# Kernel tuning notes

Measured on AMD Instinct MI355X. Metric: run time of the kernel, lower is better.

Reference implementation:

```python
import jax, jax.numpy as jnp
import numpy as np

N_AA = 20          # size of 'ACDEFGHIKLMNPQRSTVWY'
GAP = 20           # gap token; one_hot maps it to an all-zero row (matches '-' skipping)
N_SEQS, SEQ_LEN = 2048, 512
MAX_MI_POS = 100   # min(seq_len, 100) in the source
PSEUDOCOUNT = 0.01


def _features(msa, pc):
    n_seqs, seq_len = msa.shape
    pseudocount = PSEUDOCOUNT * pc[0]

    # one-hot encode; tokens >= N_AA (gaps / unknown) become zero rows,
    # exactly matching the 'if aa in self.aa_to_idx' / "aa != '-'" skips.
    oh = jax.nn.one_hot(msa, N_AA, dtype=jnp.float32)          # [N, L, 20]

    # ---- PSSM ----
    counts = oh.sum(0)                                          # [L, 20]
    freq = (counts + pseudocount) / (n_seqs + pseudocount * N_AA)
    pssm = jnp.log(freq * N_AA + 1e-10)                         # log(freq / (1/20) + 1e-10)

    # ---- Conservation (Shannon entropy over non-gap residues) ----
    total = counts.sum(-1, keepdims=True)                       # [L, 1] non-gap count
    f = counts / jnp.maximum(total, 1.0)
    # f == 0 terms contribute 0 * log2(1e-10) == 0, matching dict-based skipping
    entropy = -(f * jnp.log2(f + 1e-10)).sum(-1)                # [L]
    conservation = jnp.where(total[:, 0] > 0,
                             1.0 - entropy / np.log2(N_AA), 0.0)

    # ---- Mutual information over the first M positions ----
    M = min(seq_len, MAX_MI_POS)
    ohm = oh[:, :M, :]                                          # [N, M, 20]
    # joint counts over sequences where BOTH positions are non-gap
    J = jnp.einsum('nia,njb->ijab', ohm, ohm)                   # [M, M, 20, 20]
    tot = J.sum((2, 3))                                         # [M, M]
    tot_safe = jnp.maximum(tot, 1.0)
    p = J / tot_safe[:, :, None, None]                          # joint prob p_ij
    pi = p.sum(3)[:, :, :, None]                                # marginal p_i (pair-conditioned)
    pj = p.sum(2)[:, :, None, :]                                # marginal p_j
    denom = jnp.maximum(pi * pj, 1e-30)
    term = jnp.where(J > 0, p * jnp.log2(p / denom + 1e-10), 0.0)
    mi = jnp.where(tot > 0, term.sum((2, 3)), 0.0)              # [M, M]
    mi = mi * (1.0 - jnp.eye(M, dtype=mi.dtype))                # diagonal left at 0
    mi_matrix = jnp.zeros((seq_len, seq_len), jnp.float32).at[:M, :M].set(mi)

    return pssm, conservation, mi_matrix


def setup_inputs() -> dict:
    key = jax.random.key(0)
    k1, _ = jax.random.split(key)
    # tokens 0..19 = amino acids, 20 = gap '-'
    msa = jax.random.randint(k1, (N_SEQS, SEQ_LEN), 0, N_AA + 1, dtype=jnp.int32)
    pc = jnp.ones((1,), dtype=jnp.float32)  # pseudocount scale (==1 -> pseudocount 0.01)
    return {"msa": msa, "pc": pc}


def reference(msa, pc):
    return _features(msa, pc)
```

## Files before the change

kernel.cpp:

```cpp
#include <hip/hip_runtime.h>

#define N_SEQS 2048
#define SEQ_LEN 512
#define NAA 20
#define NS 21
#define MPOS 100
#define G 4
#define NG (MPOS / G)
#define NTILE (NG * (NG + 1) / 2)
#define POSB (SEQ_LEN / 8)
#define HBINS (NS * NS)

__global__ __launch_bounds__(256) void fused_kernel(const int* __restrict__ msa,
                                                    const float* __restrict__ pc,
                                                    float* __restrict__ pssm,
                                                    float* __restrict__ cons,
                                                    float* __restrict__ mi) {
    __shared__ int h_s[16 * HBINS];
    __shared__ float ra_s[4][NAA], cb_s[4][NAA];

    const int tid = threadIdx.x;
    const int w = tid >> 6;
    const int lane = tid & 63;
    const int bid = blockIdx.x;

    if (bid < NTILE) {
        int t = bid, ti = 0, off = 0;
        while (off + (NG - ti) <= t) { off += NG - ti; ++ti; }
        const int tj = ti + (t - off);
        const int i0 = ti * G, j0 = tj * G;
        const bool diag = (ti == tj);

        for (int k = tid; k < 16 * HBINS; k += 256) h_s[k] = 0;
        __syncthreads();

#pragma unroll
        for (int k = 0; k < 8; ++k) {
            const int s = tid + (k << 8);
            const int* rp = msa + (size_t)s * SEQ_LEN;
            const int4 va = *(const int4*)(rp + i0);
            const int4 vb = *(const int4*)(rp + j0);
            const int A0 = va.x * 21, A1 = va.y * 21, A2 = va.z * 21, A3 = va.w * 21;
            const int B0 = vb.x, B1 = vb.y, B2 = vb.z, B3 = vb.w;
            atomicAdd(&h_s[0 * 1764 + 0 * 441 + A0 + B0], 1);
            atomicAdd(&h_s[0 * 1764 + 1 * 441 + A0 + B1], 1);
            atomicAdd(&h_s[0 * 1764 + 2 * 441 + A0 + B2], 1);
            atomicAdd(&h_s[0 * 1764 + 3 * 441 + A0 + B3], 1);
            atomicAdd(&h_s[1 * 1764 + 0 * 441 + A1 + B0], 1);
            atomicAdd(&h_s[1 * 1764 + 1 * 441 + A1 + B1], 1);
            atomicAdd(&h_s[1 * 1764 + 2 * 441 + A1 + B2], 1);
            atomicAdd(&h_s[1 * 1764 + 3 * 441 + A1 + B3], 1);
            atomicAdd(&h_s[2 * 1764 + 0 * 441 + A2 + B0], 1);
            atomicAdd(&h_s[2 * 1764 + 1 * 441 + A2 + B1], 1);
            atomicAdd(&h_s[2 * 1764 + 2 * 441 + A2 + B2], 1);
            atomicAdd(&h_s[2 * 1764 + 3 * 441 + A2 + B3], 1);
            atomicAdd(&h_s[3 * 1764 + 0 * 441 + A3 + B0], 1);
            atomicAdd(&h_s[3 * 1764 + 1 * 441 + A3 + B1], 1);
            atomicAdd(&h_s[3 * 1764 + 2 * 441 + A3 + B2], 1);
            atomicAdd(&h_s[3 * 1764 + 3 * 441 + A3 + B3], 1);
        }
        __syncthreads();

#pragma unroll
        for (int q = 0; q < 4; ++q) {
            const int p = w * 4 + q;
            const int pi = p >> 2, pj = p & 3;
            if (diag && pi >= pj) continue;
            const int* h = h_s + p * HBINS;

            if (lane < NAA) {
                int s = 0;
#pragma unroll
                for (int b = 0; b < NAA; ++b) s += h[lane * NS + b];
                ra_s[w][lane] = (float)s;
            } else if (lane >= 32 && lane < 32 + NAA) {
                int c = lane - 32, s = 0;
#pragma unroll
                for (int a = 0; a < NAA; ++a) s += h[a * NS + c];
                cb_s[w][c] = (float)s;
            }

            float tot = 0.f;
#pragma unroll
            for (int a = 0; a < NAA; ++a) tot += ra_s[w][a];
            const float ts = fmaxf(tot, 1.f);
            const float inv = __fdividef(1.f, ts);

            float part = 0.f;
#pragma unroll
            for (int u = 0; u < 7; ++u) {
                const int k = lane + 64 * u;
                if (k < NAA * NAA) {
                    const int row = k / NAA;
                    const int col = k - row * NAA;
                    const int J = h[row * NS + col];
                    if (J > 0) {
                        float pp = (float)J * inv;
                        float pi_f = ra_s[w][row] * inv;
                        float pj_f = cb_s[w][col] * inv;
                        float denom = fmaxf(pi_f * pj_f, 1e-30f);
                        part += pp * __log2f(__fdividef(pp, denom) + 1e-10f);
                    }
                }
            }
#pragma unroll
            for (int o = 32; o; o >>= 1) part += __shfl_down(part, o, 64);

            if (lane == 0) {
                const float m = (tot > 0.f) ? part : 0.f;
                mi[(size_t)(i0 + pi) * SEQ_LEN + (j0 + pj)] = m;
                mi[(size_t)(j0 + pj) * SEQ_LEN + (i0 + pi)] = m;
            }
        }
    } else {
        const int pb = bid - NTILE;
        const int i0 = pb * 8;

        for (int r = 0; r < 8; ++r) {
            const int i = i0 + r;
            float* rowp = mi + (size_t)i * SEQ_LEN;
            if (i < MPOS) {
                for (int c = MPOS + tid; c < SEQ_LEN; c += 256) rowp[c] = 0.f;
                if (tid == 0) rowp[i] = 0.f;
            } else {
                if (tid < SEQ_LEN / 4)
                    ((float4*)rowp)[tid] = make_float4(0.f, 0.f, 0.f, 0.f);
            }
        }

        for (int k = tid; k < 4 * 8 * NS; k += 256) h_s[k] = 0;
        __syncthreads();

        int* h = h_s + w * (8 * NS);
#pragma unroll
        for (int k = 0; k < 8; ++k) {
            const int s = tid + (k << 8);
            const int* rp = msa + (size_t)s * SEQ_LEN + i0;
            const int4 v0 = *(const int4*)rp;
            const int4 v1 = *(const int4*)(rp + 4);
            atomicAdd(&h[0 * NS + v0.x], 1);
            atomicAdd(&h[1 * NS + v0.y], 1);
            atomicAdd(&h[2 * NS + v0.z], 1);
            atomicAdd(&h[3 * NS + v0.w], 1);
            atomicAdd(&h[4 * NS + v1.x], 1);
            atomicAdd(&h[5 * NS + v1.y], 1);
            atomicAdd(&h[6 * NS + v1.z], 1);
            atomicAdd(&h[7 * NS + v1.w], 1);
        }
        __syncthreads();

        float* cntf = (float*)(h_s + 1024);
        if (tid < 8 * NAA) {
            const int p = tid / NAA, a = tid - p * NAA;
            const int idx = p * NS + a;
            const int c = h_s[idx] + h_s[168 + idx] + h_s[336 + idx] + h_s[504 + idx];
            cntf[tid] = (float)c;
            const float pcnt = 0.01f * pc[0];
            const float freq = __fdividef((float)c + pcnt, 2048.0f + pcnt * 20.0f);
            pssm[(size_t)(i0 + p) * NAA + a] = __logf(freq * 20.0f + 1e-10f);
        }
        __syncthreads();

        const int p = tid >> 5, l = tid & 31;
        const float fc = (l < NAA) ? cntf[p * NAA + l] : 0.f;
        float tt = fc;
#pragma unroll
        for (int o = 16; o; o >>= 1) tt += __shfl_xor(tt, o, 32);
        const float ts2 = fmaxf(tt, 1.f);
        const float f = __fdividef(fc, ts2);
        float term = (l < NAA) ? -f * __log2f(f + 1e-10f) : 0.f;
#pragma unroll
        for (int o = 16; o; o >>= 1) term += __shfl_xor(term, o, 32);
        if (l == 0)
            cons[i0 + p] = (tt > 0.f) ? (1.f - term * 0.2313782131597592f) : 0.f;
    }
}

extern "C" void kernel_launch(void* const* d_in, const int* in_sizes, int n_in,
                              void* d_out, int out_size, void* d_ws, size_t ws_size,
                              hipStream_t stream) {
    const int* msa = (const int*)d_in[0];
    const float* pc = (const float*)d_in[1];

    float* pssm = (float*)d_out;
    float* cons = pssm + SEQ_LEN * NAA;
    float* mi = cons + SEQ_LEN;

    fused_kernel<<<NTILE + POSB, 256, 0, stream>>>(msa, pc, pssm, cons, mi);
}
```

Measured before the change: 19.64 us.

## Split into packing/position kernel and MI kernel with byte-transposed columns and 5x5 tiles

Splits the fused kernel into two launches. The first computes PSSM and conservation and also writes the first 100 MSA columns as a transposed byte array into workspace. The second builds joint histograms for 5x5 position tiles from coalesced packed byte loads. The MI formula is rewritten algebraically as sum J log J minus the marginal terms, normalised by the total, which removes the per-bin divisions. In exchange it adds a second launch, a serial dependency between the kernels, and 25 pair histograms per block (about 44KB of LDS), which lowers occupancy.

```diff
diff --git a/kernel.cpp b/kernel.cpp
--- a/kernel.cpp
+++ b/kernel.cpp
@@ -5,174 +5,214 @@
 #define NAA 20
 #define NS 21
 #define MPOS 100
-#define G 4
-#define NG (MPOS / G)
-#define NTILE (NG * (NG + 1) / 2)
-#define POSB (SEQ_LEN / 8)
-#define HBINS (NS * NS)
-
-__global__ __launch_bounds__(256) void fused_kernel(const int* __restrict__ msa,
-                                                    const float* __restrict__ pc,
-                                                    float* __restrict__ pssm,
-                                                    float* __restrict__ cons,
-                                                    float* __restrict__ mi) {
-    __shared__ int h_s[16 * HBINS];
-    __shared__ float ra_s[4][NAA], cb_s[4][NAA];
-
+#define G 5
+#define NG 20
+#define NTILE 210
+#define HB (NS * NS)
+#define POSB 64
+
+__global__ __launch_bounds__(256) void pos_kernel(const int* __restrict__ msa,
+                                                  const float* __restrict__ pc,
+                                                  unsigned char* __restrict__ cols,
+                                                  int do_pack,
+                                                  float* __restrict__ pssm,
+                                                  float* __restrict__ cons,
+                                                  float* __restrict__ mi) {
+    __shared__ int ph[4][8 * NS];
+    __shared__ float cntf[8 * NAA];
+    const int tid = threadIdx.x;
+    const int w = tid >> 6;
+    const int i0 = blockIdx.x * 8;
+
+    for (int r = 0; r < 8; ++r) {
+        const int i = i0 + r;
+        float* rowp = mi + (size_t)i * SEQ_LEN;
+        if (i < MPOS) {
+            for (int c = MPOS + tid; c < SEQ_LEN; c += 256) rowp[c] = 0.f;
+            if (tid == 0) rowp[i] = 0.f;
+        } else {
+            if (tid < SEQ_LEN / 4)
+                ((float4*)rowp)[tid] = make_float4(0.f, 0.f, 0.f, 0.f);
+        }
+    }
+
+    for (int k = tid; k < 4 * 8 * NS; k += 256) ((int*)ph)[k] = 0;
+    __syncthreads();
+
+    int* h = ph[w];
+#pragma unroll
+    for (int k = 0; k < 8; ++k) {
+        const int s = tid + (k << 8);
+        const int* rp = msa + (size_t)s * SEQ_LEN + i0;
+        const int4 v0 = *(const int4*)rp;
+        const int4 v1 = *(const int4*)(rp + 4);
+        if (do_pack && i0 < MPOS) {
+            if (i0 + 0 < MPOS) cols[(size_t)(i0 + 0) * N_SEQS + s] = (unsigned char)v0.x;
+            if (i0 + 1 < MPOS) cols[(size_t)(i0 + 1) * N_SEQS + s] = (unsigned char)v0.y;
+            if (i0 + 2 < MPOS) cols[(size_t)(i0 + 2) * N_SEQS + s] = (unsigned char)v0.z;
+            if (i0 + 3 < MPOS) cols[(size_t)(i0 + 3) * N_SEQS + s] = (unsigned char)v0.w;
+            if (i0 + 4 < MPOS) cols[(size_t)(i0 + 4) * N_SEQS + s] = (unsigned char)v1.x;
+            if (i0 + 5 < MPOS) cols[(size_t)(i0 + 5) * N_SEQS + s] = (unsigned char)v1.y;
+            if (i0 + 6 < MPOS) cols[(size_t)(i0 + 6) * N_SEQS + s] = (unsigned char)v1.z;
+            if (i0 + 7 < MPOS) cols[(size_t)(i0 + 7) * N_SEQS + s] = (unsigned char)v1.w;
+        }
+        atomicAdd(&h[0 * NS + v0.x], 1);
+        atomicAdd(&h[1 * NS + v0.y], 1);
+        atomicAdd(&h[2 * NS + v0.z], 1);
+        atomicAdd(&h[3 * NS + v0.w], 1);
+        atomicAdd(&h[4 * NS + v1.x], 1);
+        atomicAdd(&h[5 * NS + v1.y], 1);
+        atomicAdd(&h[6 * NS + v1.z], 1);
+        atomicAdd(&h[7 * NS + v1.w], 1);
+    }
+    __syncthreads();
+
+    if (tid < 8 * NAA) {
+        const int p = tid / NAA, a = tid - p * NAA;
+        const int idx = p * NS + a;
+        const int c = ph[0][idx] + ph[1][idx] + ph[2][idx] + ph[3][idx];
+        cntf[tid] = (float)c;
+        const float pcnt = 0.01f * pc[0];
+        const float freq = __fdividef((float)c + pcnt, 2048.0f + pcnt * 20.0f);
+        pssm[(size_t)(i0 + p) * NAA + a] = __logf(freq * 20.0f + 1e-10f);
+    }
+    __syncthreads();
+
+    const int p = tid >> 5, l = tid & 31;
+    const float fc = (l < NAA) ? cntf[p * NAA + l] : 0.f;
+    float tt = fc;
+#pragma unroll
+    for (int o = 16; o; o >>= 1) tt += __shfl_xor(tt, o, 32);
+    const float ts2 = fmaxf(tt, 1.f);
+    const float f = __fdividef(fc, ts2);
+    float term = (l < NAA) ? -f * __log2f(f + 1e-10f) : 0.f;
+#pragma unroll
+    for (int o = 16; o; o >>= 1) term += __shfl_xor(term, o, 32);
+    if (l == 0)
+        cons[i0 + p] = (tt > 0.f) ? (1.f - term * 0.2313782131597592f) : 0.f;
+}
+
+__global__ __launch_bounds__(256) void mi_kernel(const int* __restrict__ msa,
+                                                 const unsigned char* __restrict__ cols,
+                                                 int use_pack,
+                                                 float* __restrict__ mi) {
+    __shared__ int h_s[G * G * HB];
     const int tid = threadIdx.x;
     const int w = tid >> 6;
     const int lane = tid & 63;
-    const int bid = blockIdx.x;
-
-    if (bid < NTILE) {
-        int t = bid, ti = 0, off = 0;
-        while (off + (NG - ti) <= t) { off += NG - ti; ++ti; }
-        const int tj = ti + (t - off);
-        const int i0 = ti * G, j0 = tj * G;
-        const bool diag = (ti == tj);
-
-        for (int k = tid; k < 16 * HBINS; k += 256) h_s[k] = 0;
-        __syncthreads();
-
-#pragma unroll
+
+    int t = blockIdx.x, ti = 0, off = 0;
+    while (off + (NG - ti) <= t) { off += NG - ti; ++ti; }
+    const int tj = ti + (t - off);
+    const int i0 = ti * G, j0 = tj * G;
+    const bool diag = (ti == tj);
+
+    for (int k = tid; k < G * G * HB; k += 256) h_s[k] = 0;
+    __syncthreads();
+
+    if (use_pack) {
+#pragma unroll
+        for (int pass = 0; pass < 2; ++pass) {
+            const int s4 = pass * 1024 + tid * 4;
+            const unsigned int ua0 = *(const unsigned int*)(cols + (size_t)(i0 + 0) * N_SEQS + s4);
+            const unsigned int ua1 = *(const unsigned int*)(cols + (size_t)(i0 + 1) * N_SEQS + s4);
+            const unsigned int ua2 = *(const unsigned int*)(cols + (size_t)(i0 + 2) * N_SEQS + s4);
+            const unsigned int ua3 = *(const unsigned int*)(cols + (size_t)(i0 + 3) * N_SEQS + s4);
+            const unsigned int ua4 = *(const unsigned int*)(cols + (size_t)(i0 + 4) * N_SEQS + s4);
+            const unsigned int ub0 = *(const unsigned int*)(cols + (size_t)(j0 + 0) * N_SEQS + s4);
+            const unsigned int ub1 = *(const unsigned int*)(cols + (size_t)(j0 + 1) * N_SEQS + s4);
+            const unsigned int ub2 = *(const unsigned int*)(cols + (size_t)(j0 + 2) * N_SEQS + s4);
+            const unsigned int ub3 = *(const unsigned int*)(cols + (size_t)(j0 + 3) * N_SEQS + s4);
+            const unsigned int ub4 = *(const unsigned int*)(cols + (size_t)(j0 + 4) * N_SEQS + s4);
+#pragma unroll
+            for (int q = 0; q < 4; ++q) {
+                const int sh = 8 * q;
+                const int A0 = (int)((ua0 >> sh) & 0xFF) * NS;
+                const int A1 = (int)((ua1 >> sh) & 0xFF) * NS;
+                const int A2 = (int)((ua2 >> sh) & 0xFF) * NS;
+                const int A3 = (int)((ua3 >> sh) & 0xFF) * NS;
+                const int A4 = (int)((ua4 >> sh) & 0xFF) * NS;
+                const int B0 = (int)((ub0 >> sh) & 0xFF);
+                const int B1 = (int)((ub1 >> sh) & 0xFF);
+                const int B2 = (int)((ub2 >> sh) & 0xFF);
+                const int B3 = (int)((ub3 >> sh) & 0xFF);
+                const int B4 = (int)((ub4 >> sh) & 0xFF);
+#define UPD(PI, PJ, AA, BB) atomicAdd(&h_s[(PI * G + PJ) * HB + AA + BB], 1)
+                UPD(0, 0, A0, B0); UPD(0, 1, A0, B1); UPD(0, 2, A0, B2); UPD(0, 3, A0, B3); UPD(0, 4, A0, B4);
+                UPD(1, 0, A1, B0); UPD(1, 1, A1, B1); UPD(1, 2, A1, B2); UPD(1, 3, A1, B3); UPD(1, 4, A1, B4);
+                UPD(2, 0, A2, B0); UPD(2, 1, A2, B1); UPD(2, 2, A2, B2); UPD(2, 3, A2, B3); UPD(2, 4, A2, B4);
+                UPD(3, 0, A3, B0); UPD(3, 1, A3, B1); UPD(3, 2, A3, B2); UPD(3, 3, A3, B3); UPD(3, 4, A3, B4);
+                UPD(4, 0, A4, B0); UPD(4, 1, A4, B1); UPD(4, 2, A4, B2); UPD(4, 3, A4, B3); UPD(4, 4, A4, B4);
+#undef UPD
+            }
+        }
+    } else {
         for (int k = 0; k < 8; ++k) {
             const int s = tid + (k << 8);
             const int* rp = msa + (size_t)s * SEQ_LEN;
-            const int4 va = *(const int4*)(rp + i0);
-            const int4 vb = *(const int4*)(rp + j0);
-            const int A0 = va.x * 21, A1 = va.y * 21, A2 = va.z * 21, A3 = va.w * 21;
-            const int B0 = vb.x, B1 = vb.y, B2 = vb.z, B3 = vb.w;
-            atomicAdd(&h_s[0 * 1764 + 0 * 441 + A0 + B0], 1);
-            atomicAdd(&h_s[0 * 1764 + 1 * 441 + A0 + B1], 1);
-            atomicAdd(&h_s[0 * 1764 + 2 * 441 + A0 + B2], 1);
-            atomicAdd(&h_s[0 * 1764 + 3 * 441 + A0 + B3], 1);
-            atomicAdd(&h_s[1 * 1764 + 0 * 441 + A1 + B0], 1);
-            atomicAdd(&h_s[1 * 1764 + 1 * 441 + A1 + B1], 1);
-            atomicAdd(&h_s[1 * 1764 + 2 * 441 + A1 + B2], 1);
-            atomicAdd(&h_s[1 * 1764 + 3 * 441 + A1 + B3], 1);
-            atomicAdd(&h_s[2 * 1764 + 0 * 441 + A2 + B0], 1);
-            atomicAdd(&h_s[2 * 1764 + 1 * 441 + A2 + B1], 1);
-            atomicAdd(&h_s[2 * 1764 + 2 * 441 + A2 + B2], 1);
-            atomicAdd(&h_s[2 * 1764 + 3 * 441 + A2 + B3], 1);
-            atomicAdd(&h_s[3 * 1764 + 0 * 441 + A3 + B0], 1);
-            atomicAdd(&h_s[3 * 1764 + 1 * 441 + A3 + B1], 1);
-            atomicAdd(&h_s[3 * 1764 + 2 * 441 + A3 + B2], 1);
-            atomicAdd(&h_s[3 * 1764 + 3 * 441 + A3 + B3], 1);
-        }
-        __syncthreads();
-
-#pragma unroll
-        for (int q = 0; q < 4; ++q) {
-            const int p = w * 4 + q;
-            const int pi = p >> 2, pj = p & 3;
-            if (diag && pi >= pj) continue;
-            const int* h = h_s + p * HBINS;
-
-            if (lane < NAA) {
-                int s = 0;
-#pragma unroll
-                for (int b = 0; b < NAA; ++b) s += h[lane * NS + b];
-                ra_s[w][lane] = (float)s;
-            } else if (lane >= 32 && lane < 32 + NAA) {
-                int c = lane - 32, s = 0;
-#pragma unroll
-                for (int a = 0; a < NAA; ++a) s += h[a * NS + c];
-                cb_s[w][c] = (float)s;
-            }
-
-            float tot = 0.f;
-#pragma unroll
-            for (int a = 0; a < NAA; ++a) tot += ra_s[w][a];
-            const float ts = fmaxf(tot, 1.f);
-            const float inv = __fdividef(1.f, ts);
-
-            float part = 0.f;
-#pragma unroll
-            for (int u = 0; u < 7; ++u) {
-                const int k = lane + 64 * u;
-                if (k < NAA * NAA) {
-                    const int row = k / NAA;
-                    const int col = k - row * NAA;
-                    const int J = h[row * NS + col];
-                    if (J > 0) {
-                        float pp = (float)J * inv;
-                        float pi_f = ra_s[w][row] * inv;
-                        float pj_f = cb_s[w][col] * inv;
-                        float denom = fmaxf(pi_f * pj_f, 1e-30f);
-                        part += pp * __log2f(__fdividef(pp, denom) + 1e-10f);
-                    }
+            const int A0 = rp[i0 + 0] * NS, A1 = rp[i0 + 1] * NS, A2 = rp[i0 + 2] * NS,
+                      A3 = rp[i0 + 3] * NS, A4 = rp[i0 + 4] * NS;
+            const int B0 = rp[j0 + 0], B1 = rp[j0 + 1], B2 = rp[j0 + 2],
+                      B3 = rp[j0 + 3], B4 = rp[j0 + 4];
+#define UPD(PI, PJ, AA, BB) atomicAdd(&h_s[(PI * G + PJ) * HB + AA + BB], 1)
+            UPD(0, 0, A0, B0); UPD(0, 1, A0, B1); UPD(0, 2, A0, B2); UPD(0, 3, A0, B3); UPD(0, 4, A0, B4);
+            UPD(1, 0, A1, B0); UPD(1, 1, A1, B1); UPD(1, 2, A1, B2); UPD(1, 3, A1, B3); UPD(1, 4, A1, B4);
+            UPD(2, 0, A2, B0); UPD(2, 1, A2, B1); UPD(2, 2, A2, B2); UPD(2, 3, A2, B3); UPD(2, 4, A2, B4);
+            UPD(3, 0, A3, B0); UPD(3, 1, A3, B1); UPD(3, 2, A3, B2); UPD(3, 3, A3, B3); UPD(3, 4, A3, B4);
+            UPD(4, 0, A4, B0); UPD(4, 1, A4, B1); UPD(4, 2, A4, B2); UPD(4, 3, A4, B3); UPD(4, 4, A4, B4);
+#undef UPD
+        }
+    }
+    __syncthreads();
+
+    for (int p = w; p < G * G; p += 4) {
+        const int pi = p / G, pj = p - (p / G) * G;
+        if (diag && pi >= pj) continue;
+        const int* h = h_s + p * HB;
+
+        float mterm = 0.f, tpart = 0.f;
+        if (lane < NAA) {
+            int s = 0;
+#pragma unroll
+            for (int b = 0; b < NAA; ++b) s += h[lane * NS + b];
+            const float R = (float)s;
+            tpart = R;
+            if (s > 0) mterm = R * __log2f(R);
+        } else if (lane >= 32 && lane < 32 + NAA) {
+            const int c = lane - 32;
+            int s = 0;
+#pragma unroll
+            for (int a = 0; a < NAA; ++a) s += h[a * NS + c];
+            const float C = (float)s;
+            if (s > 0) mterm = C * __log2f(C);
+        }
+
+        float part = -mterm;
+#pragma unroll
+        for (int u = 0; u < 7; ++u) {
+            const int k2 = lane + (u << 6);
+            if (k2 < NAA * NAA) {
+                const int row = k2 / NAA;
+                const int col = k2 - row * NAA;
+                const int J = h[row * NS + col];
+                if (J > 0) {
+                    const float fJ = (float)J;
+                    part += fJ * __log2f(fJ);
                 }
             }
-#pragma unroll
-            for (int o = 32; o; o >>= 1) part += __shfl_down(part, o, 64);
-
-            if (lane == 0) {
-                const float m = (tot > 0.f) ? part : 0.f;
-                mi[(size_t)(i0 + pi) * SEQ_LEN + (j0 + pj)] = m;
-                mi[(size_t)(j0 + pj) * SEQ_LEN + (i0 + pi)] = m;
-            }
-        }
-    } else {
-        const int pb = bid - NTILE;
-        const int i0 = pb * 8;
-
-        for (int r = 0; r < 8; ++r) {
-            const int i = i0 + r;
-            float* rowp = mi + (size_t)i * SEQ_LEN;
-            if (i < MPOS) {
-                for (int c = MPOS + tid; c < SEQ_LEN; c += 256) rowp[c] = 0.f;
-                if (tid == 0) rowp[i] = 0.f;
-            } else {
-                if (tid < SEQ_LEN / 4)
-                    ((float4*)rowp)[tid] = make_float4(0.f, 0.f, 0.f, 0.f);
-            }
-        }
-
-        for (int k = tid; k < 4 * 8 * NS; k += 256) h_s[k] = 0;
-        __syncthreads();
-
-        int* h = h_s + w * (8 * NS);
-#pragma unroll
-        for (int k = 0; k < 8; ++k) {
-            const int s = tid + (k << 8);
-            const int* rp = msa + (size_t)s * SEQ_LEN + i0;
-            const int4 v0 = *(const int4*)rp;
-            const int4 v1 = *(const int4*)(rp + 4);
-            atomicAdd(&h[0 * NS + v0.x], 1);
-            atomicAdd(&h[1 * NS + v0.y], 1);
-            atomicAdd(&h[2 * NS + v0.z], 1);
-            atomicAdd(&h[3 * NS + v0.w], 1);
-            atomicAdd(&h[4 * NS + v1.x], 1);
-            atomicAdd(&h[5 * NS + v1.y], 1);
-            atomicAdd(&h[6 * NS + v1.z], 1);
-            atomicAdd(&h[7 * NS + v1.w], 1);
-        }
-        __syncthreads();
-
-        float* cntf = (float*)(h_s + 1024);
-        if (tid < 8 * NAA) {
-            const int p = tid / NAA, a = tid - p * NAA;
-            const int idx = p * NS + a;
-            const int c = h_s[idx] + h_s[168 + idx] + h_s[336 + idx] + h_s[504 + idx];
-            cntf[tid] = (float)c;
-            const float pcnt = 0.01f * pc[0];
-            const float freq = __fdividef((float)c + pcnt, 2048.0f + pcnt * 20.0f);
-            pssm[(size_t)(i0 + p) * NAA + a] = __logf(freq * 20.0f + 1e-10f);
-        }
-        __syncthreads();
-
-        const int p = tid >> 5, l = tid & 31;
-        const float fc = (l < NAA) ? cntf[p * NAA + l] : 0.f;
-        float tt = fc;
-#pragma unroll
-        for (int o = 16; o; o >>= 1) tt += __shfl_xor(tt, o, 32);
-        const float ts2 = fmaxf(tt, 1.f);
-        const float f = __fdividef(fc, ts2);
-        float term = (l < NAA) ? -f * __log2f(f + 1e-10f) : 0.f;
-#pragma unroll
-        for (int o = 16; o; o >>= 1) term += __shfl_xor(term, o, 32);
-        if (l == 0)
-            cons[i0 + p] = (tt > 0.f) ? (1.f - term * 0.2313782131597592f) : 0.f;
+        }
+#pragma unroll
+        for (int o = 32; o; o >>= 1) {
+            part += __shfl_down(part, o, 64);
+            tpart += __shfl_down(tpart, o, 64);
+        }
+        if (lane == 0) {
+            const float m = (tpart > 0.f)
+                                ? __fdividef(part, tpart) + __log2f(tpart)
+                                : 0.f;
+            mi[(size_t)(i0 + pi) * SEQ_LEN + (j0 + pj)] = m;
+            mi[(size_t)(j0 + pj) * SEQ_LEN + (i0 + pi)] = m;
+        }
     }
 }
 
@@ -186,5 +226,9 @@
     float* cons = pssm + SEQ_LEN * NAA;
     float* mi = cons + SEQ_LEN;
 
-    fused_kernel<<<NTILE + POSB, 256, 0, stream>>>(msa, pc, pssm, cons, mi);
+    unsigned char* cols = (unsigned char*)d_ws;
+    const int do_pack = (ws_size >= (size_t)MPOS * N_SEQS) ? 1 : 0;
+
+    pos_kernel<<<POSB, 256, 0, stream>>>(msa, pc, cols, do_pack, pssm, cons, mi);
+    mi_kernel<<<NTILE, 256, 0, stream>>>(msa, cols, do_pack, mi);
 }
```

Result: slower. 24.54 us (+25.0%).

## Use 512-thread blocks with split histograms and count-based MI formula

Applied to the files above, without the earlier changes.

Doubles block size to 512 threads and gives each half of the block its own private joint histogram, which halves LDS atomic contention and per-thread sequence loads. The two copies are summed during the MI step. Mutual information is rewritten algebraically as (sum J log J - sum R log R - sum C log C)/T + log T on raw counts, which removes the per-bin divisions and the shared marginal arrays. The PSSM blocks use 8 per-wave histograms. The cost is twice the shared memory per block, and the closed form may differ slightly from the reference in float rounding.

```diff
diff --git a/kernel.cpp b/kernel.cpp
--- a/kernel.cpp
+++ b/kernel.cpp
@@ -6,18 +6,18 @@
 #define NS 21
 #define MPOS 100
 #define G 4
-#define NG (MPOS / G)
-#define NTILE (NG * (NG + 1) / 2)
-#define POSB (SEQ_LEN / 8)
-#define HBINS (NS * NS)
+#define NG 25
+#define NTILE 325
+#define HB (NS * NS)
+#define POSB 64
+#define NBLK (NTILE + POSB)
 
-__global__ __launch_bounds__(256) void fused_kernel(const int* __restrict__ msa,
+__global__ __launch_bounds__(512) void fused_kernel(const int* __restrict__ msa,
                                                     const float* __restrict__ pc,
                                                     float* __restrict__ pssm,
                                                     float* __restrict__ cons,
                                                     float* __restrict__ mi) {
-    __shared__ int h_s[16 * HBINS];
-    __shared__ float ra_s[4][NAA], cb_s[4][NAA];
+    __shared__ int h_s[2 * 16 * HB];
 
     const int tid = threadIdx.x;
     const int w = tid >> 6;
@@ -31,83 +31,82 @@
         const int i0 = ti * G, j0 = tj * G;
         const bool diag = (ti == tj);
 
-        for (int k = tid; k < 16 * HBINS; k += 256) h_s[k] = 0;
+        for (int k = tid; k < 2 * 16 * HB; k += 512) h_s[k] = 0;
         __syncthreads();
 
+        const int half = tid >> 8;
+        const int htid = tid & 255;
+        int* H = h_s + half * (16 * HB);
 #pragma unroll
-        for (int k = 0; k < 8; ++k) {
-            const int s = tid + (k << 8);
+        for (int k = 0; k < 4; ++k) {
+            const int s = half * 1024 + htid + (k << 8);
             const int* rp = msa + (size_t)s * SEQ_LEN;
             const int4 va = *(const int4*)(rp + i0);
             const int4 vb = *(const int4*)(rp + j0);
-            const int A0 = va.x * 21, A1 = va.y * 21, A2 = va.z * 21, A3 = va.w * 21;
-            const int B0 = vb.x, B1 = vb.y, B2 = vb.z, B3 = vb.w;
-            atomicAdd(&h_s[0 * 1764 + 0 * 441 + A0 + B0], 1);
-            atomicAdd(&h_s[0 * 1764 + 1 * 441 + A0 + B1], 1);
-            atomicAdd(&h_s[0 * 1764 + 2 * 441 + A0 + B2], 1);
-            atomicAdd(&h_s[0 * 1764 + 3 * 441 + A0 + B3], 1);
-            atomicAdd(&h_s[1 * 1764 + 0 * 441 + A1 + B0], 1);
-            atomicAdd(&h_s[1 * 1764 + 1 * 441 + A1 + B1], 1);
-            atomicAdd(&h_s[1 * 1764 + 2 * 441 + A1 + B2], 1);
-            atomicAdd(&h_s[1 * 1764 + 3 * 441 + A1 + B3], 1);
-            atomicAdd(&h_s[2 * 1764 + 0 * 441 + A2 + B0], 1);
-            atomicAdd(&h_s[2 * 1764 + 1 * 441 + A2 + B1], 1);
-            atomicAdd(&h_s[2 * 1764 + 2 * 441 + A2 + B2], 1);
-            atomicAdd(&h_s[2 * 1764 + 3 * 441 + A2 + B3], 1);
-            atomicAdd(&h_s[3 * 1764 + 0 * 441 + A3 + B0], 1);
-            atomicAdd(&h_s[3 * 1764 + 1 * 441 + A3 + B1], 1);
-            atomicAdd(&h_s[3 * 1764 + 2 * 441 + A3 + B2], 1);
-            atomicAdd(&h_s[3 * 1764 + 3 * 441 + A3 + B3], 1);
+            const int A0 = va.x * NS, A1 = va.y * NS, A2 = va.z * NS, A3 = va.w * NS;
+#define UPD(PI, PJ, AA, BB) atomicAdd(&H[(PI * 4 + PJ) * HB + AA + BB], 1)
+            UPD(0, 0, A0, vb.x); UPD(0, 1, A0, vb.y); UPD(0, 2, A0, vb.z); UPD(0, 3, A0, vb.w);
+            UPD(1, 0, A1, vb.x); UPD(1, 1, A1, vb.y); UPD(1, 2, A1, vb.z); UPD(1, 3, A1, vb.w);
+            UPD(2, 0, A2, vb.x); UPD(2, 1, A2, vb.y); UPD(2, 2, A2, vb.z); UPD(2, 3, A2, vb.w);
+            UPD(3, 0, A3, vb.x); UPD(3, 1, A3, vb.y); UPD(3, 2, A3, vb.z); UPD(3, 3, A3, vb.w);
+#undef UPD
         }
         __syncthreads();
 
 #pragma unroll
-        for (int q = 0; q < 4; ++q) {
-            const int p = w * 4 + q;
+        for (int q = 0; q < 2; ++q) {
+            const int p = w * 2 + q;
             const int pi = p >> 2, pj = p & 3;
             if (diag && pi >= pj) continue;
-            const int* h = h_s + p * HBINS;
+            const int* hA = h_s + p * HB;
+            const int* hB = h_s + 16 * HB + p * HB;
 
+            float mterm = 0.f, tpart = 0.f;
             if (lane < NAA) {
                 int s = 0;
 #pragma unroll
-                for (int b = 0; b < NAA; ++b) s += h[lane * NS + b];
-                ra_s[w][lane] = (float)s;
+                for (int b = 0; b < NAA; ++b)
+                    s += hA[lane * NS + b] + hB[lane * NS + b];
+                if (s > 0) {
+                    const float R = (float)s;
+                    tpart = R;
+                    mterm = R * __log2f(R);
+                }
             } else if (lane >= 32 && lane < 32 + NAA) {
-                int c = lane - 32, s = 0;
+                const int c = lane - 32;
+                int s = 0;
 #pragma unroll
-                for (int a = 0; a < NAA; ++a) s += h[a * NS + c];
-                cb_s[w][c] = (float)s;
+                for (int a = 0; a < NAA; ++a)
+                    s += hA[a * NS + c] + hB[a * NS + c];
+                if (s > 0) {
+                    const float C = (float)s;
+                    mterm = C * __log2f(C);
+                }
             }
 
-            float tot = 0.f;
-#pragma unroll
-            for (int a = 0; a < NAA; ++a) tot += ra_s[w][a];
-            const float ts = fmaxf(tot, 1.f);
-            const float inv = __fdividef(1.f, ts);
-
-            float part = 0.f;
+            float part = -mterm;
 #pragma unroll
             for (int u = 0; u < 7; ++u) {
-                const int k = lane + 64 * u;
-                if (k < NAA * NAA) {
-                    const int row = k / NAA;
-                    const int col = k - row * NAA;
-                    const int J = h[row * NS + col];
+                const int k2 = lane + (u << 6);
+                if (k2 < NAA * NAA) {
+                    const int row = k2 / NAA;
+                    const int col = k2 - row * NAA;
+                    const int J = hA[row * NS + col] + hB[row * NS + col];
                     if (J > 0) {
-                        float pp = (float)J * inv;
-                        float pi_f = ra_s[w][row] * inv;
-                        float pj_f = cb_s[w][col] * inv;
-                        float denom = fmaxf(pi_f * pj_f, 1e-30f);
-                        part += pp * __log2f(__fdividef(pp, denom) + 1e-10f);
+                        const float fJ = (float)J;
+                        part += fJ * __log2f(fJ);
                     }
                 }
             }
 #pragma unroll
-            for (int o = 32; o; o >>= 1) part += __shfl_down(part, o, 64);
-
+            for (int o = 32; o; o >>= 1) {
+                part += __shfl_down(part, o, 64);
+                tpart += __shfl_down(tpart, o, 64);
+            }
             if (lane == 0) {
-                const float m = (tot > 0.f) ? part : 0.f;
+                const float m = (tpart > 0.f)
+                                    ? __fdividef(part, tpart) + __log2f(tpart)
+                                    : 0.f;
                 mi[(size_t)(i0 + pi) * SEQ_LEN + (j0 + pj)] = m;
                 mi[(size_t)(j0 + pj) * SEQ_LEN + (i0 + pi)] = m;
             }
@@ -120,7 +119,8 @@
             const int i = i0 + r;
             float* rowp = mi + (size_t)i * SEQ_LEN;
             if (i < MPOS) {
-                for (int c = MPOS + tid; c < SEQ_LEN; c += 256) rowp[c] = 0.f;
+                const int c = MPOS + tid;
+                if (c < SEQ_LEN) rowp[c] = 0.f;
                 if (tid == 0) rowp[i] = 0.f;
             } else {
                 if (tid < SEQ_LEN / 4)
@@ -128,13 +128,13 @@
             }
         }
 
-        for (int k = tid; k < 4 * 8 * NS; k += 256) h_s[k] = 0;
+        for (int k = tid; k < 8 * 8 * NS; k += 512) h_s[k] = 0;
         __syncthreads();
 
         int* h = h_s + w * (8 * NS);
 #pragma unroll
-        for (int k = 0; k < 8; ++k) {
-            const int s = tid + (k << 8);
+        for (int k = 0; k < 4; ++k) {
+            const int s = tid + (k << 9);
             const int* rp = msa + (size_t)s * SEQ_LEN + i0;
             const int4 v0 = *(const int4*)rp;
             const int4 v1 = *(const int4*)(rp + 4);
@@ -149,11 +149,13 @@
         }
         __syncthreads();
 
-        float* cntf = (float*)(h_s + 1024);
+        float* cntf = (float*)(h_s + 2048);
         if (tid < 8 * NAA) {
             const int p = tid / NAA, a = tid - p * NAA;
             const int idx = p * NS + a;
-            const int c = h_s[idx] + h_s[168 + idx] + h_s[336 + idx] + h_s[504 + idx];
+            int c = 0;
+#pragma unroll
+            for (int ww = 0; ww < 8; ++ww) c += h_s[ww * (8 * NS) + idx];
             cntf[tid] = (float)c;
             const float pcnt = 0.01f * pc[0];
             const float freq = __fdividef((float)c + pcnt, 2048.0f + pcnt * 20.0f);
@@ -161,18 +163,20 @@
         }
         __syncthreads();
 
-        const int p = tid >> 5, l = tid & 31;
-        const float fc = (l < NAA) ? cntf[p * NAA + l] : 0.f;
-        float tt = fc;
+        if (tid < 256) {
+            const int p = tid >> 5, l = tid & 31;
+            const float fc = (l < NAA) ? cntf[p * NAA + l] : 0.f;
+            float tt = fc;
 #pragma unroll
-        for (int o = 16; o; o >>= 1) tt += __shfl_xor(tt, o, 32);
-        const float ts2 = fmaxf(tt, 1.f);
-        const float f = __fdividef(fc, ts2);
-        float term = (l < NAA) ? -f * __log2f(f + 1e-10f) : 0.f;
+            for (int o = 16; o; o >>= 1) tt += __shfl_xor(tt, o, 32);
+            const float ts2 = fmaxf(tt, 1.f);
+            const float f = __fdividef(fc, ts2);
+            float term = (l < NAA) ? -f * __log2f(f + 1e-10f) : 0.f;
 #pragma unroll
-        for (int o = 16; o; o >>= 1) term += __shfl_xor(term, o, 32);
-        if (l == 0)
-            cons[i0 + p] = (tt > 0.f) ? (1.f - term * 0.2313782131597592f) : 0.f;
+            for (int o = 16; o; o >>= 1) term += __shfl_xor(term, o, 32);
+            if (l == 0)
+                cons[i0 + p] = (tt > 0.f) ? (1.f - term * 0.2313782131597592f) : 0.f;
+        }
     }
 }
 
@@ -186,5 +190,5 @@
     float* cons = pssm + SEQ_LEN * NAA;
     float* mi = cons + SEQ_LEN;
 
-    fused_kernel<<<NTILE + POSB, 256, 0, stream>>>(msa, pc, pssm, cons, mi);
+    fused_kernel<<<NBLK, 512, 0, stream>>>(msa, pc, pssm, cons, mi);
 }
```

Result: faster. 17.94 us (-8.6%).
